# Kernel optimization log

Hardware: AMD Instinct MI355X
Metric: run time of the kernel (lower is better)

Reference implementation:

```python
import jax, jax.numpy as jnp
import numpy as np

D_MODEL = 768; N_LAYERS = 4; SOC_WINDOW = 10
D_INNER = 2 * D_MODEL; D_STATE = 16; DT_RANK = D_MODEL // 16; D_CONV = 4
EPS = 1e-5
B, T = 4, 1024


def setup_inputs() -> dict:
    key = jax.random.key(0)
    ks = jax.random.split(key, 10)
    w = lambda k, s, sc=0.02: jax.random.normal(k, s, jnp.float32) * sc
    return {
        "x": jax.random.normal(ks[0], (B, T, 2 + SOC_WINDOW), jnp.float32),
        "inp_w": w(ks[1], (D_MODEL, 2 + SOC_WINDOW)),
        "inp_b": jnp.zeros((D_MODEL,), jnp.float32),
        "in_proj_w": w(ks[2], (N_LAYERS, 2 * D_INNER, D_MODEL)),
        "conv_w": w(ks[3], (N_LAYERS, D_INNER, D_CONV), 0.1),
        "conv_b": jnp.zeros((N_LAYERS, D_INNER), jnp.float32),
        "x_proj_w": w(ks[4], (N_LAYERS, DT_RANK + 2 * D_STATE, D_INNER)),
        "dt_proj_w": w(ks[5], (N_LAYERS, D_INNER, DT_RANK), 0.05),
        "dt_proj_b": w(ks[6], (N_LAYERS, D_INNER), 0.5),
        "A_log": jnp.tile(jnp.log(jnp.arange(1.0, D_STATE + 1.0, dtype=jnp.float32)), (N_LAYERS, D_INNER, 1)),
        "D_skip": jnp.ones((N_LAYERS, D_INNER), jnp.float32),
        "out_proj_w": w(ks[7], (N_LAYERS, D_MODEL, D_INNER)),
        "ln_w": jnp.ones((N_LAYERS, D_MODEL), jnp.float32),
        "norm_w": jnp.ones((D_MODEL,), jnp.float32),
        "head_w": w(ks[8], (1, D_MODEL)),
        "head_b": jnp.zeros((1,), jnp.float32),
    }


def _rmsnorm(x, w):
    return x * jax.lax.rsqrt(jnp.mean(x * x, axis=-1, keepdims=True) + EPS) * w


def _mamba_block(x, in_w, cw, cb, xp_w, dtw, dtb, A_log, Dsk, out_w):
    Bsz = x.shape[0]
    xz = jnp.einsum('btd,ed->bte', x, in_w)            # (B,T,2*D_INNER)
    xx, z = jnp.split(xz, 2, axis=-1)
    # causal depthwise conv1d (pad left d_conv-1, truncate to T)
    xc = jax.lax.conv_general_dilated(
        jnp.swapaxes(xx, 1, 2), cw[:, None, :], (1,), [(D_CONV - 1, 0)],
        feature_group_count=D_INNER, dimension_numbers=('NCH', 'OIH', 'NCH'))
    xx = jax.nn.silu(jnp.swapaxes(xc + cb[None, :, None], 1, 2))  # (B,T,D_INNER)
    dbc = jnp.einsum('btd,ed->bte', xx, xp_w)          # (B,T,dt_rank+2*N)
    delta = jax.nn.softplus(jnp.einsum('btr,dr->btd', dbc[..., :DT_RANK], dtw) + dtb)
    Bm = dbc[..., DT_RANK:DT_RANK + D_STATE]           # (B,T,N)
    Cm = dbc[..., DT_RANK + D_STATE:]                  # (B,T,N)
    A = -jnp.exp(A_log)                                # (D_INNER,N)

    def step(h, inp):
        d_t, x_t, b_t, c_t = inp                       # (B,Din),(B,Din),(B,N),(B,N)
        h = jnp.exp(d_t[..., None] * A) * h + (d_t * x_t)[..., None] * b_t[:, None, :]
        return h, jnp.einsum('bdn,bn->bd', h, c_t)

    h0 = jnp.zeros((Bsz, D_INNER, D_STATE), x.dtype)
    _, ys = jax.lax.scan(step, h0, (jnp.moveaxis(delta, 1, 0), jnp.moveaxis(xx, 1, 0),
                                    jnp.moveaxis(Bm, 1, 0), jnp.moveaxis(Cm, 1, 0)))
    y = jnp.moveaxis(ys, 0, 1) + Dsk * xx
    y = y * jax.nn.silu(z)
    return jnp.einsum('bte,de->btd', y, out_w)


def reference(x, inp_w, inp_b, in_proj_w, conv_w, conv_b, x_proj_w, dt_proj_w, dt_proj_b,
              A_log, D_skip, out_proj_w, ln_w, norm_w, head_w, head_b):
    h = jnp.einsum('btf,df->btd', x, inp_w) + inp_b
    for l in range(N_LAYERS):
        h = h + _mamba_block(_rmsnorm(h, ln_w[l]), in_proj_w[l], conv_w[l], conv_b[l],
                             x_proj_w[l], dt_proj_w[l], dt_proj_b[l], A_log[l],
                             D_skip[l], out_proj_w[l])
    h = _rmsnorm(h, norm_w)
    y = jnp.einsum('btd,od->bto', h, head_w) + head_b
    return y[..., 0]
```

## Files before the change

kernel.cpp:

```cpp
#include <hip/hip_runtime.h>
#include <stdint.h>

#define D_MODEL   768
#define D_INNER   1536
#define D_STATE   16
#define DT_RANK   48
#define NB        4
#define TSEQ      1024
#define NTOK      4096
#define EPS       1e-5f
#define CHUNK     32
#define NCHUNK    32
#define XP_N      128

typedef __bf16 bf16;
typedef __bf16 bf16x8 __attribute__((ext_vector_type(8)));
typedef float  floatx4 __attribute__((ext_vector_type(4)));

__device__ __forceinline__ float silu_f(float v)     { return v / (1.f + __expf(-v)); }
__device__ __forceinline__ float softplus_f(float v) { return v > 20.f ? v : __logf(1.f + __expf(v)); }

__device__ __forceinline__ void async_ld16(const void* g, void* l) {
  __builtin_amdgcn_global_load_lds((__attribute__((address_space(1))) uint32_t*)g,
                                   (__attribute__((address_space(3))) uint32_t*)l, 16, 0, 0);
}

__global__ __launch_bounds__(256) void prep_k(const float* __restrict__ win, const float* __restrict__ wout,
                                              bf16* __restrict__ bin, bf16* __restrict__ bout) {
  const int i = blockIdx.x * 256 + threadIdx.x;
  const int NIN = 4 * 3072 * 768;
  if (i < NIN) bin[i] = (bf16)win[i];
  else         bout[i - NIN] = (bf16)wout[i - NIN];
}

__global__ __launch_bounds__(256) void prep_xp_k(const float* __restrict__ w, bf16* __restrict__ wb) {
  const int i = blockIdx.x * 256 + threadIdx.x;
  const int k = i % 1536;
  const int r = (i / 1536) % XP_N;
  const int l = i / (1536 * XP_N);
  wb[i] = (r < 80) ? (bf16)w[((size_t)l * 80 + r) * 1536 + k] : (bf16)0.f;
}

__global__ __launch_bounds__(256) void input_proj_k(const float* __restrict__ x, const float* __restrict__ w,
                                                    const float* __restrict__ bvec, float* __restrict__ h) {
  const int idx = blockIdx.x * 256 + threadIdx.x;
  const int d = idx % D_MODEL;
  const int t = idx / D_MODEL;
  float acc = bvec[d];
  #pragma unroll
  for (int f = 0; f < 12; ++f) acc = fmaf(x[t * 12 + f], w[d * 12 + f], acc);
  h[idx] = acc;
}

__global__ __launch_bounds__(256) void rmsnorm_k(const float* __restrict__ h, const float* __restrict__ lnw,
                                                 bf16* __restrict__ xn) {
  const int t = blockIdx.x;
  const float* __restrict__ hr = h + (size_t)t * D_MODEL;
  float v[3];
  float ss = 0.f;
  #pragma unroll
  for (int i = 0; i < 3; ++i) { v[i] = hr[threadIdx.x + i * 256]; ss = fmaf(v[i], v[i], ss); }
  #pragma unroll
  for (int o = 32; o > 0; o >>= 1) ss += __shfl_down(ss, o, 64);
  __shared__ float red[4];
  if ((threadIdx.x & 63) == 0) red[threadIdx.x >> 6] = ss;
  __syncthreads();
  const float tot = red[0] + red[1] + red[2] + red[3];
  const float rs = rsqrtf(tot / (float)D_MODEL + EPS);
  #pragma unroll
  for (int i = 0; i < 3; ++i) {
    const int d = threadIdx.x + i * 256;
    xn[(size_t)t * D_MODEL + d] = (bf16)(v[i] * rs * lnw[d]);
  }
}

template <int MODE>
__global__ __launch_bounds__(256) void gemm_bt(const bf16* __restrict__ A, const bf16* __restrict__ B,
                                               void* __restrict__ Cv, const int N, const int K, const int kLen) {
  alignas(16) __shared__ bf16 As[128 * 32];
  alignas(16) __shared__ bf16 Bs[128 * 32];
  const int tid = threadIdx.x;
  const int lane = tid & 63;
  const int wid = tid >> 6;
  const int wm = wid & 1, wn = wid >> 1;
  const int m0 = blockIdx.x * 128, n0 = blockIdx.y * 128;
  const int kOff = blockIdx.z * kLen;

  floatx4 acc[4][4];
  #pragma unroll
  for (int i = 0; i < 4; ++i)
    #pragma unroll
    for (int j = 0; j < 4; ++j) acc[i][j] = (floatx4){0.f, 0.f, 0.f, 0.f};

  const int srow = lane >> 2;
  const int skp  = (lane & 3) * 8;
  const int fr = lane & 15;
  const int fk = (lane >> 4) * 8;

  for (int k0 = 0; k0 < kLen; k0 += 32) {
    __syncthreads();
    #pragma unroll
    for (int i = 0; i < 2; ++i) {
      const int seg = wid * 2 + i;
      const int row = seg * 16 + srow;
      async_ld16(A + (size_t)(m0 + row) * K + kOff + k0 + skp, (char*)As + seg * 1024);
      async_ld16(B + (size_t)(n0 + row) * K + kOff + k0 + skp, (char*)Bs + seg * 1024);
    }
    __syncthreads();
    bf16x8 a[4], b[4];
    #pragma unroll
    for (int t = 0; t < 4; ++t) {
      a[t] = *(const bf16x8*)&As[(wm * 64 + t * 16 + fr) * 32 + fk];
      b[t] = *(const bf16x8*)&Bs[(wn * 64 + t * 16 + fr) * 32 + fk];
    }
    #pragma unroll
    for (int i = 0; i < 4; ++i)
      #pragma unroll
      for (int j = 0; j < 4; ++j)
        acc[i][j] = __builtin_amdgcn_mfma_f32_16x16x32_bf16(a[i], b[j], acc[i][j], 0, 0, 0);
  }

  const int quad = lane >> 4, col = lane & 15;
  #pragma unroll
  for (int i = 0; i < 4; ++i)
    #pragma unroll
    for (int j = 0; j < 4; ++j) {
      const int gm0 = m0 + wm * 64 + i * 16 + quad * 4;
      const int gn  = n0 + wn * 64 + j * 16 + col;
      #pragma unroll
      for (int r = 0; r < 4; ++r) {
        const size_t off = (size_t)(gm0 + r) * N + gn;
        const float v = acc[i][j][r];
        if (MODE == 0)      ((float*)Cv)[off] = v;
        else if (MODE == 1) ((bf16*)Cv)[off] = (bf16)v;
        else                atomicAdd(&((float*)Cv)[off], v);
      }
    }
}

__global__ __launch_bounds__(256) void conv_silu_k(const bf16* __restrict__ xz, const float* __restrict__ cw,
                                                   const float* __restrict__ cb, bf16* __restrict__ xxb) {
  const int idx = blockIdx.x * 256 + threadIdx.x;
  const int d = idx % D_INNER;
  const int bt = idx / D_INNER;
  const int t = bt & (TSEQ - 1);
  float acc = cb[d];
  #pragma unroll
  for (int j = 0; j < 4; ++j) {
    const int tt = t - 3 + j;
    if (tt >= 0) acc = fmaf((float)xz[(size_t)(bt - 3 + j) * (2 * D_INNER) + d], cw[d * 4 + j], acc);
  }
  xxb[idx] = (bf16)silu_f(acc);
}

__global__ __launch_bounds__(256) void scan_p1_k(const bf16* __restrict__ xxb, const float* __restrict__ dbc,
                                                 const float* __restrict__ dtw, const float* __restrict__ dtb,
                                                 const float* __restrict__ Alog,
                                                 float* __restrict__ S, float* __restrict__ su,
                                                 float* __restrict__ delta) {
  const int c = blockIdx.x;
  const int d = blockIdx.y * 256 + threadIdx.x;
  const int b = blockIdx.z;
  float w[DT_RANK];
  #pragma unroll
  for (int k = 0; k < DT_RANK; k += 4) {
    const float4 t4 = *(const float4*)&dtw[(size_t)d * DT_RANK + k];
    w[k] = t4.x; w[k + 1] = t4.y; w[k + 2] = t4.z; w[k + 3] = t4.w;
  }
  const float bias = dtb[d];
  float A[16], Sv[16];
  bool fast = true;
  #pragma unroll
  for (int n = 0; n < 16; ++n) {
    A[n] = -__expf(Alog[(size_t)d * 16 + n]);
    fast = fast && (__builtin_fabsf(A[n] + (float)(n + 1)) < 1e-3f);
    Sv[n] = 0.f;
  }
  float sus = 0.f;
  const int bt0 = b * TSEQ + c * CHUNK;
  if (fast) {
    for (int tt = 0; tt < CHUNK; ++tt) {
      const size_t bt = bt0 + tt;
      const float* __restrict__ db = dbc + bt * XP_N;
      float dacc = bias;
      #pragma unroll
      for (int k = 0; k < DT_RANK; ++k) dacc = fmaf(db[k], w[k], dacc);
      const float du = softplus_f(dacc);
      delta[bt * D_INNER + d] = du;
      sus += du;
      const float xv  = (float)xxb[bt * D_INNER + d];
      const float dux = du * xv;
      const float* __restrict__ Bp = db + DT_RANK;
      const float r = __expf(-du);
      float e = r;
      #pragma unroll
      for (int n = 0; n < 16; ++n) {
        Sv[n] = fmaf(e, Sv[n], dux * Bp[n]);
        e *= r;
      }
    }
  } else {
    for (int tt = 0; tt < CHUNK; ++tt) {
      const size_t bt = bt0 + tt;
      const float* __restrict__ db = dbc + bt * XP_N;
      float dacc = bias;
      #pragma unroll
      for (int k = 0; k < DT_RANK; ++k) dacc = fmaf(db[k], w[k], dacc);
      const float du = softplus_f(dacc);
      delta[bt * D_INNER + d] = du;
      sus += du;
      const float xv  = (float)xxb[bt * D_INNER + d];
      const float dux = du * xv;
      const float* __restrict__ Bp = db + DT_RANK;
      #pragma unroll
      for (int n = 0; n < 16; ++n)
        Sv[n] = fmaf(__expf(du * A[n]), Sv[n], dux * Bp[n]);
    }
  }
  const size_t base = ((size_t)(b * NCHUNK + c) * 16) * D_INNER + d;
  #pragma unroll
  for (int n = 0; n < 16; ++n) S[base + (size_t)n * D_INNER] = Sv[n];
  su[(size_t)(b * NCHUNK + c) * D_INNER + d] = sus;
}

__global__ __launch_bounds__(256) void scan_fold_k(const float* __restrict__ Alog, const float* __restrict__ su,
                                                   float* __restrict__ S) {
  const int idx = blockIdx.x * 256 + threadIdx.x;
  const int d = idx % D_INNER;
  const int bn = idx / D_INNER;
  const int n = bn & 15;
  const int b = bn >> 4;
  const float A = -__expf(Alog[(size_t)d * 16 + n]);
  float H = 0.f;
  #pragma unroll 4
  for (int c = 0; c < NCHUNK; ++c) {
    const size_t off = ((size_t)((b * NCHUNK + c) * 16 + n)) * D_INNER + d;
    const float Pv = __expf(A * su[(size_t)(b * NCHUNK + c) * D_INNER + d]);
    const float Sv = S[off];
    S[off] = H;
    H = fmaf(Pv, H, Sv);
  }
}

__global__ __launch_bounds__(256) void scan_p3_k(const bf16* __restrict__ xxb, const float* __restrict__ dbc,
                                                 const float* __restrict__ delta, const float* __restrict__ Alog,
                                                 const float* __restrict__ Hin,
                                                 const bf16* __restrict__ xz, const float* __restrict__ Dsk,
                                                 bf16* __restrict__ yg) {
  const int c = blockIdx.x;
  const int d = blockIdx.y * 256 + threadIdx.x;
  const int b = blockIdx.z;
  const size_t hbase = ((size_t)(b * NCHUNK + c) * 16) * D_INNER + d;
  float A[16], H[16];
  bool fast = true;
  #pragma unroll
  for (int n = 0; n < 16; ++n) {
    A[n] = -__expf(Alog[(size_t)d * 16 + n]);
    fast = fast && (__builtin_fabsf(A[n] + (float)(n + 1)) < 1e-3f);
    H[n] = Hin[hbase + (size_t)n * D_INNER];
  }
  const float dsk = Dsk[d];
  const int bt0 = b * TSEQ + c * CHUNK;
  if (fast) {
    for (int tt = 0; tt < CHUNK; ++tt) {
      const size_t bt = bt0 + tt;
      const float du  = delta[bt * D_INNER + d];
      const float xv  = (float)xxb[bt * D_INNER + d];
      const float dux = du * xv;
      const float* __restrict__ db = dbc + bt * XP_N;
      const float* __restrict__ Bp = db + DT_RANK;
      const float* __restrict__ Cp = db + DT_RANK + 16;
      const float r = __expf(-du);
      float e = r, y = 0.f;
      #pragma unroll
      for (int n = 0; n < 16; ++n) {
        H[n] = fmaf(e, H[n], dux * Bp[n]);
        y = fmaf(H[n], Cp[n], y);
        e *= r;
      }
      const float z = (float)xz[bt * (2 * D_INNER) + D_INNER + d];
      yg[bt * D_INNER + d] = (bf16)((y + dsk * xv) * silu_f(z));
    }
  } else {
    for (int tt = 0; tt < CHUNK; ++tt) {
      const size_t bt = bt0 + tt;
      const float du  = delta[bt * D_INNER + d];
      const float xv  = (float)xxb[bt * D_INNER + d];
      const float dux = du * xv;
      const float* __restrict__ db = dbc + bt * XP_N;
      const float* __restrict__ Bp = db + DT_RANK;
      const float* __restrict__ Cp = db + DT_RANK + 16;
      float y = 0.f;
      #pragma unroll
      for (int n = 0; n < 16; ++n) {
        H[n] = fmaf(__expf(du * A[n]), H[n], dux * Bp[n]);
        y = fmaf(H[n], Cp[n], y);
      }
      const float z = (float)xz[bt * (2 * D_INNER) + D_INNER + d];
      yg[bt * D_INNER + d] = (bf16)((y + dsk * xv) * silu_f(z));
    }
  }
}

__global__ __launch_bounds__(256) void final_k(const float* __restrict__ h, const float* __restrict__ nw,
                                               const float* __restrict__ hw, const float* __restrict__ hb,
                                               float* __restrict__ out) {
  const int t = blockIdx.x;
  const float* __restrict__ hr = h + (size_t)t * D_MODEL;
  float ss = 0.f, dt_ = 0.f;
  #pragma unroll
  for (int i = 0; i < 3; ++i) {
    const int d = threadIdx.x + i * 256;
    const float v = hr[d];
    ss  = fmaf(v, v, ss);
    dt_ = fmaf(v, nw[d] * hw[d], dt_);
  }
  #pragma unroll
  for (int o = 32; o > 0; o >>= 1) { ss += __shfl_down(ss, o, 64); dt_ += __shfl_down(dt_, o, 64); }
  __shared__ float r0[4], r1[4];
  if ((threadIdx.x & 63) == 0) { r0[threadIdx.x >> 6] = ss; r1[threadIdx.x >> 6] = dt_; }
  __syncthreads();
  if (threadIdx.x == 0) {
    const float sst = r0[0] + r0[1] + r0[2] + r0[3];
    const float dtt = r1[0] + r1[1] + r1[2] + r1[3];
    out[t] = dtt * rsqrtf(sst / (float)D_MODEL + EPS) + hb[0];
  }
}

extern "C" void kernel_launch(void* const* d_in, const int* in_sizes, int n_in,
                              void* d_out, int out_size, void* d_ws, size_t ws_size,
                              hipStream_t stream) {
  (void)in_sizes; (void)n_in; (void)out_size; (void)ws_size;
  const float* x     = (const float*)d_in[0];
  const float* inpw  = (const float*)d_in[1];
  const float* inpb  = (const float*)d_in[2];
  const float* inprj = (const float*)d_in[3];
  const float* convw = (const float*)d_in[4];
  const float* convb = (const float*)d_in[5];
  const float* xprjw = (const float*)d_in[6];
  const float* dtw   = (const float*)d_in[7];
  const float* dtb   = (const float*)d_in[8];
  const float* alog  = (const float*)d_in[9];
  const float* dskip = (const float*)d_in[10];
  const float* outw  = (const float*)d_in[11];
  const float* lnw   = (const float*)d_in[12];
  const float* normw = (const float*)d_in[13];
  const float* headw = (const float*)d_in[14];
  const float* headb = (const float*)d_in[15];
  float* out = (float*)d_out;

  char* p = (char*)d_ws;
  auto take = [&](size_t bytes) { char* q = p; p += (bytes + 255) & ~(size_t)255; return q; };
  bf16*  wbin  = (bf16*) take((size_t)4 * 3072 * 768 * 2);
  bf16*  wbout = (bf16*) take((size_t)4 * 768 * 1536 * 2);
  bf16*  wbxp  = (bf16*) take((size_t)4 * XP_N * 1536 * 2);
  float* h     = (float*)take((size_t)NTOK * D_MODEL * 4);
  bf16*  xn    = (bf16*) take((size_t)NTOK * D_MODEL * 2);
  bf16*  xzb   = (bf16*) take((size_t)NTOK * 2 * D_INNER * 2);
  bf16*  xxb   = (bf16*) take((size_t)NTOK * D_INNER * 2);
  float* dbc   = (float*)take((size_t)NTOK * XP_N * 4);
  float* dlt   = (float*)take((size_t)NTOK * D_INNER * 4);
  float* Sb    = (float*)take((size_t)NB * NCHUNK * 16 * D_INNER * 4);
  float* su    = (float*)take((size_t)NB * NCHUNK * D_INNER * 4);
  bf16*  yg    = (bf16*) take((size_t)NTOK * D_INNER * 2);

  prep_k<<<55296, 256, 0, stream>>>(inprj, outw, wbin, wbout);
  prep_xp_k<<<4 * XP_N * 1536 / 256, 256, 0, stream>>>(xprjw, wbxp);
  input_proj_k<<<NTOK * D_MODEL / 256, 256, 0, stream>>>(x, inpw, inpb, h);

  for (int l = 0; l < 4; ++l) {
    rmsnorm_k<<<NTOK, 256, 0, stream>>>(h, lnw + l * D_MODEL, xn);
    gemm_bt<1><<<dim3(32, 24, 1), 256, 0, stream>>>(xn, wbin + (size_t)l * 3072 * 768, xzb, 3072, 768, 768);
    conv_silu_k<<<NTOK * D_INNER / 256, 256, 0, stream>>>(xzb, convw + l * D_INNER * 4, convb + l * D_INNER, xxb);
    hipMemsetAsync(dbc, 0, (size_t)NTOK * XP_N * 4, stream);
    gemm_bt<2><<<dim3(32, 1, 4), 256, 0, stream>>>(xxb, wbxp + (size_t)l * XP_N * 1536, dbc, XP_N, 1536, 384);
    scan_p1_k<<<dim3(NCHUNK, 6, NB), 256, 0, stream>>>(xxb, dbc, dtw + (size_t)l * D_INNER * DT_RANK,
                                                       dtb + l * D_INNER, alog + (size_t)l * D_INNER * 16,
                                                       Sb, su, dlt);
    scan_fold_k<<<NB * 16 * D_INNER / 256, 256, 0, stream>>>(alog + (size_t)l * D_INNER * 16, su, Sb);
    scan_p3_k<<<dim3(NCHUNK, 6, NB), 256, 0, stream>>>(xxb, dbc, dlt, alog + (size_t)l * D_INNER * 16,
                                                       Sb, xzb, dskip + l * D_INNER, yg);
    gemm_bt<2><<<dim3(32, 6, 2), 256, 0, stream>>>(yg, wbout + (size_t)l * 768 * 1536, h, 768, 1536, 768);
  }

  final_k<<<NTOK, 256, 0, stream>>>(h, normw, headw, headb, out);
}
```

Measured before the change: 867.4 us.

## Fuse prep kernels, fold memset into conv, packed-fp32 scans, retune split-K

Merges the three setup kernels into one launch and moves the dbc zeroing into the conv_silu kernel, removing a memset and two launches per run. The scan kernels are rewritten to use two-wide float vectors so the compiler can emit packed FP32 FMA instructions for the state recurrence and the delta projection. Split-K factors are raised for the x_proj GEMM (4 to 8) and the out_proj GEMM (2 to 3) to spread work over more blocks. The cost is more atomic adds into the outputs and a vector reduction order that differs slightly from the scalar one.

```diff
diff --git a/kernel.cpp b/kernel.cpp
--- a/kernel.cpp
+++ b/kernel.cpp
@@ -16,6 +16,7 @@
 typedef __bf16 bf16;
 typedef __bf16 bf16x8 __attribute__((ext_vector_type(8)));
 typedef float  floatx4 __attribute__((ext_vector_type(4)));
+typedef float  f32x2   __attribute__((ext_vector_type(2)));
 
 __device__ __forceinline__ float silu_f(float v)     { return v / (1.f + __expf(-v)); }
 __device__ __forceinline__ float softplus_f(float v) { return v > 20.f ? v : __logf(1.f + __expf(v)); }
@@ -26,30 +27,32 @@
 }
 
 __global__ __launch_bounds__(256) void prep_k(const float* __restrict__ win, const float* __restrict__ wout,
-                                              bf16* __restrict__ bin, bf16* __restrict__ bout) {
-  const int i = blockIdx.x * 256 + threadIdx.x;
-  const int NIN = 4 * 3072 * 768;
-  if (i < NIN) bin[i] = (bf16)win[i];
-  else         bout[i - NIN] = (bf16)wout[i - NIN];
-}
-
-__global__ __launch_bounds__(256) void prep_xp_k(const float* __restrict__ w, bf16* __restrict__ wb) {
-  const int i = blockIdx.x * 256 + threadIdx.x;
-  const int k = i % 1536;
-  const int r = (i / 1536) % XP_N;
-  const int l = i / (1536 * XP_N);
-  wb[i] = (r < 80) ? (bf16)w[((size_t)l * 80 + r) * 1536 + k] : (bf16)0.f;
-}
-
-__global__ __launch_bounds__(256) void input_proj_k(const float* __restrict__ x, const float* __restrict__ w,
-                                                    const float* __restrict__ bvec, float* __restrict__ h) {
-  const int idx = blockIdx.x * 256 + threadIdx.x;
-  const int d = idx % D_MODEL;
-  const int t = idx / D_MODEL;
-  float acc = bvec[d];
-  #pragma unroll
-  for (int f = 0; f < 12; ++f) acc = fmaf(x[t * 12 + f], w[d * 12 + f], acc);
-  h[idx] = acc;
+                                              const float* __restrict__ wxp,
+                                              const float* __restrict__ x, const float* __restrict__ inw,
+                                              const float* __restrict__ inb,
+                                              bf16* __restrict__ bin, bf16* __restrict__ bout,
+                                              bf16* __restrict__ bxp, float* __restrict__ h) {
+  const int blk = blockIdx.x;
+  if (blk < 55296) {
+    const int i = blk * 256 + threadIdx.x;
+    const int NIN = 4 * 3072 * 768;
+    if (i < NIN) bin[i] = (bf16)win[i];
+    else         bout[i - NIN] = (bf16)wout[i - NIN];
+  } else if (blk < 58368) {
+    const int i = (blk - 55296) * 256 + threadIdx.x;
+    const int k = i % 1536;
+    const int r = (i / 1536) % XP_N;
+    const int l = i / (1536 * XP_N);
+    bxp[i] = (r < 80) ? (bf16)wxp[((size_t)l * 80 + r) * 1536 + k] : (bf16)0.f;
+  } else {
+    const int idx = (blk - 58368) * 256 + threadIdx.x;
+    const int d = idx % D_MODEL;
+    const int t = idx / D_MODEL;
+    float acc = inb[d];
+    #pragma unroll
+    for (int f = 0; f < 12; ++f) acc = fmaf(x[t * 12 + f], inw[d * 12 + f], acc);
+    h[idx] = acc;
+  }
 }
 
 __global__ __launch_bounds__(256) void rmsnorm_k(const float* __restrict__ h, const float* __restrict__ lnw,
@@ -139,7 +142,12 @@
 }
 
 __global__ __launch_bounds__(256) void conv_silu_k(const bf16* __restrict__ xz, const float* __restrict__ cw,
-                                                   const float* __restrict__ cb, bf16* __restrict__ xxb) {
+                                                   const float* __restrict__ cb, bf16* __restrict__ xxb,
+                                                   float* __restrict__ dbc) {
+  if (blockIdx.x < 512) {
+    const int z = blockIdx.x * 256 + threadIdx.x;
+    ((float4*)dbc)[z] = (float4){0.f, 0.f, 0.f, 0.f};
+  }
   const int idx = blockIdx.x * 256 + threadIdx.x;
   const int d = idx % D_INNER;
   const int bt = idx / D_INNER;
@@ -161,65 +169,73 @@
   const int c = blockIdx.x;
   const int d = blockIdx.y * 256 + threadIdx.x;
   const int b = blockIdx.z;
-  float w[DT_RANK];
-  #pragma unroll
-  for (int k = 0; k < DT_RANK; k += 4) {
-    const float4 t4 = *(const float4*)&dtw[(size_t)d * DT_RANK + k];
-    w[k] = t4.x; w[k + 1] = t4.y; w[k + 2] = t4.z; w[k + 3] = t4.w;
+  f32x2 w2[24];
+  #pragma unroll
+  for (int k = 0; k < 12; ++k) {
+    const float4 t4 = *(const float4*)&dtw[(size_t)d * DT_RANK + k * 4];
+    w2[2 * k]     = (f32x2){t4.x, t4.y};
+    w2[2 * k + 1] = (f32x2){t4.z, t4.w};
   }
   const float bias = dtb[d];
-  float A[16], Sv[16];
+  float A[16];
   bool fast = true;
   #pragma unroll
   for (int n = 0; n < 16; ++n) {
     A[n] = -__expf(Alog[(size_t)d * 16 + n]);
     fast = fast && (__builtin_fabsf(A[n] + (float)(n + 1)) < 1e-3f);
-    Sv[n] = 0.f;
-  }
+  }
+  f32x2 S2[8];
+  #pragma unroll
+  for (int k = 0; k < 8; ++k) S2[k] = (f32x2){0.f, 0.f};
   float sus = 0.f;
   const int bt0 = b * TSEQ + c * CHUNK;
   if (fast) {
     for (int tt = 0; tt < CHUNK; ++tt) {
       const size_t bt = bt0 + tt;
       const float* __restrict__ db = dbc + bt * XP_N;
+      f32x2 acc2 = (f32x2){bias, 0.f};
+      #pragma unroll
+      for (int k = 0; k < 24; ++k) acc2 += *(const f32x2*)&db[2 * k] * w2[k];
+      const float du = softplus_f(acc2.x + acc2.y);
+      delta[bt * D_INNER + d] = du;
+      sus += du;
+      const float xv  = (float)xxb[bt * D_INNER + d];
+      const float dux = du * xv;
+      const f32x2 dux2 = (f32x2){dux, dux};
+      const float r  = __expf(-du);
+      const float rr = r * r;
+      f32x2 E = (f32x2){r, rr};
+      const f32x2 F = (f32x2){rr, rr};
+      const f32x2* __restrict__ B2 = (const f32x2*)(db + DT_RANK);
+      #pragma unroll
+      for (int k = 0; k < 8; ++k) {
+        S2[k] = E * S2[k] + dux2 * B2[k];
+        E *= F;
+      }
+    }
+  } else {
+    for (int tt = 0; tt < CHUNK; ++tt) {
+      const size_t bt = bt0 + tt;
+      const float* __restrict__ db = dbc + bt * XP_N;
       float dacc = bias;
       #pragma unroll
-      for (int k = 0; k < DT_RANK; ++k) dacc = fmaf(db[k], w[k], dacc);
+      for (int k = 0; k < 24; ++k) { dacc = fmaf(db[2*k], w2[k].x, dacc); dacc = fmaf(db[2*k+1], w2[k].y, dacc); }
       const float du = softplus_f(dacc);
       delta[bt * D_INNER + d] = du;
       sus += du;
       const float xv  = (float)xxb[bt * D_INNER + d];
       const float dux = du * xv;
       const float* __restrict__ Bp = db + DT_RANK;
-      const float r = __expf(-du);
-      float e = r;
       #pragma unroll
       for (int n = 0; n < 16; ++n) {
-        Sv[n] = fmaf(e, Sv[n], dux * Bp[n]);
-        e *= r;
+        float* sv = (float*)&S2[n >> 1];
+        sv[n & 1] = fmaf(__expf(du * A[n]), sv[n & 1], dux * Bp[n]);
       }
     }
-  } else {
-    for (int tt = 0; tt < CHUNK; ++tt) {
-      const size_t bt = bt0 + tt;
-      const float* __restrict__ db = dbc + bt * XP_N;
-      float dacc = bias;
-      #pragma unroll
-      for (int k = 0; k < DT_RANK; ++k) dacc = fmaf(db[k], w[k], dacc);
-      const float du = softplus_f(dacc);
-      delta[bt * D_INNER + d] = du;
-      sus += du;
-      const float xv  = (float)xxb[bt * D_INNER + d];
-      const float dux = du * xv;
-      const float* __restrict__ Bp = db + DT_RANK;
-      #pragma unroll
-      for (int n = 0; n < 16; ++n)
-        Sv[n] = fmaf(__expf(du * A[n]), Sv[n], dux * Bp[n]);
-    }
   }
   const size_t base = ((size_t)(b * NCHUNK + c) * 16) * D_INNER + d;
   #pragma unroll
-  for (int n = 0; n < 16; ++n) S[base + (size_t)n * D_INNER] = Sv[n];
+  for (int n = 0; n < 16; ++n) S[base + (size_t)n * D_INNER] = ((const float*)&S2[n >> 1])[n & 1];
   su[(size_t)(b * NCHUNK + c) * D_INNER + d] = sus;
 }
 
@@ -251,13 +267,14 @@
   const int d = blockIdx.y * 256 + threadIdx.x;
   const int b = blockIdx.z;
   const size_t hbase = ((size_t)(b * NCHUNK + c) * 16) * D_INNER + d;
-  float A[16], H[16];
+  float A[16];
+  f32x2 H2[8];
   bool fast = true;
   #pragma unroll
   for (int n = 0; n < 16; ++n) {
     A[n] = -__expf(Alog[(size_t)d * 16 + n]);
     fast = fast && (__builtin_fabsf(A[n] + (float)(n + 1)) < 1e-3f);
-    H[n] = Hin[hbase + (size_t)n * D_INNER];
+    ((float*)&H2[n >> 1])[n & 1] = Hin[hbase + (size_t)n * D_INNER];
   }
   const float dsk = Dsk[d];
   const int bt0 = b * TSEQ + c * CHUNK;
@@ -267,17 +284,22 @@
       const float du  = delta[bt * D_INNER + d];
       const float xv  = (float)xxb[bt * D_INNER + d];
       const float dux = du * xv;
+      const f32x2 dux2 = (f32x2){dux, dux};
       const float* __restrict__ db = dbc + bt * XP_N;
-      const float* __restrict__ Bp = db + DT_RANK;
-      const float* __restrict__ Cp = db + DT_RANK + 16;
-      const float r = __expf(-du);
-      float e = r, y = 0.f;
-      #pragma unroll
-      for (int n = 0; n < 16; ++n) {
-        H[n] = fmaf(e, H[n], dux * Bp[n]);
-        y = fmaf(H[n], Cp[n], y);
-        e *= r;
+      const f32x2* __restrict__ B2 = (const f32x2*)(db + DT_RANK);
+      const f32x2* __restrict__ C2 = (const f32x2*)(db + DT_RANK + 16);
+      const float r  = __expf(-du);
+      const float rr = r * r;
+      f32x2 E = (f32x2){r, rr};
+      const f32x2 F = (f32x2){rr, rr};
+      f32x2 y2 = (f32x2){0.f, 0.f};
+      #pragma unroll
+      for (int k = 0; k < 8; ++k) {
+        H2[k] = E * H2[k] + dux2 * B2[k];
+        y2 = H2[k] * C2[k] + y2;
+        E *= F;
       }
+      const float y = y2.x + y2.y;
       const float z = (float)xz[bt * (2 * D_INNER) + D_INNER + d];
       yg[bt * D_INNER + d] = (bf16)((y + dsk * xv) * silu_f(z));
     }
@@ -293,8 +315,9 @@
       float y = 0.f;
       #pragma unroll
       for (int n = 0; n < 16; ++n) {
-        H[n] = fmaf(__expf(du * A[n]), H[n], dux * Bp[n]);
-        y = fmaf(H[n], Cp[n], y);
+        float* hv = (float*)&H2[n >> 1];
+        hv[n & 1] = fmaf(__expf(du * A[n]), hv[n & 1], dux * Bp[n]);
+        y = fmaf(hv[n & 1], Cp[n], y);
       }
       const float z = (float)xz[bt * (2 * D_INNER) + D_INNER + d];
       yg[bt * D_INNER + d] = (bf16)((y + dsk * xv) * silu_f(z));
@@ -364,23 +387,21 @@
   float* su    = (float*)take((size_t)NB * NCHUNK * D_INNER * 4);
   bf16*  yg    = (bf16*) take((size_t)NTOK * D_INNER * 2);
 
-  prep_k<<<55296, 256, 0, stream>>>(inprj, outw, wbin, wbout);
-  prep_xp_k<<<4 * XP_N * 1536 / 256, 256, 0, stream>>>(xprjw, wbxp);
-  input_proj_k<<<NTOK * D_MODEL / 256, 256, 0, stream>>>(x, inpw, inpb, h);
+  prep_k<<<70656, 256, 0, stream>>>(inprj, outw, xprjw, x, inpw, inpb, wbin, wbout, wbxp, h);
 
   for (int l = 0; l < 4; ++l) {
     rmsnorm_k<<<NTOK, 256, 0, stream>>>(h, lnw + l * D_MODEL, xn);
     gemm_bt<1><<<dim3(32, 24, 1), 256, 0, stream>>>(xn, wbin + (size_t)l * 3072 * 768, xzb, 3072, 768, 768);
-    conv_silu_k<<<NTOK * D_INNER / 256, 256, 0, stream>>>(xzb, convw + l * D_INNER * 4, convb + l * D_INNER, xxb);
-    hipMemsetAsync(dbc, 0, (size_t)NTOK * XP_N * 4, stream);
-    gemm_bt<2><<<dim3(32, 1, 4), 256, 0, stream>>>(xxb, wbxp + (size_t)l * XP_N * 1536, dbc, XP_N, 1536, 384);
+    conv_silu_k<<<NTOK * D_INNER / 256, 256, 0, stream>>>(xzb, convw + l * D_INNER * 4, convb + l * D_INNER,
+                                                          xxb, dbc);
+    gemm_bt<2><<<dim3(32, 1, 8), 256, 0, stream>>>(xxb, wbxp + (size_t)l * XP_N * 1536, dbc, XP_N, 1536, 192);
     scan_p1_k<<<dim3(NCHUNK, 6, NB), 256, 0, stream>>>(xxb, dbc, dtw + (size_t)l * D_INNER * DT_RANK,
                                                        dtb + l * D_INNER, alog + (size_t)l * D_INNER * 16,
                                                        Sb, su, dlt);
     scan_fold_k<<<NB * 16 * D_INNER / 256, 256, 0, stream>>>(alog + (size_t)l * D_INNER * 16, su, Sb);
     scan_p3_k<<<dim3(NCHUNK, 6, NB), 256, 0, stream>>>(xxb, dbc, dlt, alog + (size_t)l * D_INNER * 16,
                                                        Sb, xzb, dskip + l * D_INNER, yg);
-    gemm_bt<2><<<dim3(32, 6, 2), 256, 0, stream>>>(yg, wbout + (size_t)l * 768 * 1536, h, 768, 1536, 768);
+    gemm_bt<2><<<dim3(32, 6, 3), 256, 0, stream>>>(yg, wbout + (size_t)l * 768 * 1536, h, 768, 1536, 512);
   }
 
   final_k<<<NTOK, 256, 0, stream>>>(h, normw, headw, headb, out);
```

Result: slower. 886.2 us (+2.2%).
